# Optimization experiments

Measured on AMD Instinct MI355X. Metric: run time of the kernel, lower is better.

Reference implementation:

```python
import jax, jax.numpy as jnp
import numpy as np

E, H, I, T = 8, 1024, 2816, 512
E4M3_MAX = 448.0  # torch.finfo(float8_e4m3fn).max


def _quantize_to_fp8(w):
    # per-tensor dynamic scaling, identical to quantize_to_fp8 in the source
    amax = jnp.max(jnp.abs(w))
    scale = jnp.maximum(amax / E4M3_MAX, 1e-12)
    fp8 = (w / scale).astype(jnp.float8_e4m3fn)
    return fp8, scale.reshape(1).astype(jnp.float32)


def setup_inputs() -> dict:
    key = jax.random.key(0)
    k1, k2, k3, k4 = jax.random.split(key, 4)
    x = jax.random.normal(k1, (T, H), jnp.float32)
    expert_idx = jax.random.randint(k2, (T,), 0, E)
    # learned 3D expert params (stored compressed as fp8 + per-tensor scale)
    w_gu = jax.random.normal(k3, (E, 2 * I, H), jnp.float32) * 0.02
    w_d = jax.random.normal(k4, (E, H, I), jnp.float32) * 0.02
    w_gu_fp8, w_gu_scale = _quantize_to_fp8(w_gu)
    w_d_fp8, w_d_scale = _quantize_to_fp8(w_d)
    return {
        "x": x,
        "expert_idx": expert_idx,
        "w_gu_fp8": w_gu_fp8,
        "w_gu_scale": w_gu_scale,
        "w_d_fp8": w_d_fp8,
        "w_d_scale": w_d_scale,
    }


def reference(x, expert_idx, w_gu_fp8, w_gu_scale, w_d_fp8, w_d_scale):
    # materialize(): dequantize fp8 -> high precision (fp8.to(dtype) * scale)
    w_gu = w_gu_fp8.astype(jnp.float32) * w_gu_scale  # [E, 2I, H]
    w_d = w_d_fp8.astype(jnp.float32) * w_d_scale     # [E, H, I]
    # inner experts forward: SwiGLU MLP per expert, top-1 routed tokens
    gu = jnp.einsum('th,efh->tef', x, w_gu)            # [T, E, 2I]
    gate, up = jnp.split(gu, 2, axis=-1)               # [T, E, I] each
    h = jax.nn.silu(gate) * up                          # [T, E, I]
    y = jnp.einsum('tei,ehi->teh', h, w_d)              # [T, E, H]
    out = y[jnp.arange(x.shape[0]), expert_idx]         # [T, H] select routed expert
    return out
```

## Files before the change

### kernel.cpp

```cpp
#include <hip/hip_runtime.h>
#include <hip/hip_bf16.h>
#include <stdint.h>

#define E_ 8
#define H_ 1024
#define I_ 2816
#define T_ 512

typedef __attribute__((ext_vector_type(4))) float f32x4;
typedef __attribute__((ext_vector_type(8))) short short8;

typedef __attribute__((address_space(1))) const unsigned GAS;
typedef __attribute__((address_space(3))) unsigned LAS;

__device__ __forceinline__ void dma16(const void* g, void* l) {
    __builtin_amdgcn_global_load_lds((GAS*)g, (LAS*)l, 16, 0, 0);
}
__device__ __forceinline__ unsigned short f2bf(float f) {
    return __builtin_bit_cast(unsigned short, __float2bfloat16(f));
}
__device__ __forceinline__ uint32_t pack_rne(float lo, float hi) {
    return (uint32_t)f2bf(lo) | ((uint32_t)f2bf(hi) << 16);
}
__device__ __forceinline__ uint32_t pack_trunc(float lo, float hi) {
    return (__builtin_bit_cast(uint32_t, hi) & 0xFFFF0000u) |
           (__builtin_bit_cast(uint32_t, lo) >> 16);
}

#define VM2() asm volatile("s_waitcnt vmcnt(2)" ::: "memory")
#define VM6() asm volatile("s_waitcnt vmcnt(6)" ::: "memory")
#define VM0() asm volatile("s_waitcnt vmcnt(0)" ::: "memory")

__global__ __launch_bounds__(256) void route_cvt(const float* __restrict__ x,
                                                 const int* __restrict__ idx,
                                                 int* __restrict__ counts,
                                                 int* __restrict__ bucket,
                                                 unsigned short* __restrict__ xg) {
    int tid = threadIdx.x;
    if (blockIdx.x == 0) {
        if (tid < E_) counts[tid] = 0;
        for (int i = tid; i < E_ * T_; i += 256) bucket[i] = 0;
        __syncthreads();
#pragma unroll
        for (int k = 0; k < 2; ++k) {
            int t = tid + k * 256;
            int e = idx[t];
            int pos = atomicAdd(counts + e, 1);
            bucket[e * T_ + pos] = t;
        }
    }
    int unit = blockIdx.x * 256 + tid;
    const float* xp = x + (size_t)unit * 8;
    float4 a = *(const float4*)xp, b = *(const float4*)(xp + 4);
    uint4 o = make_uint4(pack_rne(a.x, a.y), pack_rne(a.z, a.w),
                         pack_rne(b.x, b.y), pack_rne(b.z, b.w));
    *(uint4*)(xg + (size_t)unit * 8) = o;
}

__global__ __launch_bounds__(256) void gemm1(const unsigned short* __restrict__ xg,
                                             const float* __restrict__ wgu,
                                             const float* __restrict__ sgu_p,
                                             const int* __restrict__ counts,
                                             const int* __restrict__ bucket,
                                             __hip_bfloat16* __restrict__ hbuf) {
    int e = blockIdx.x;
    int f0 = blockIdx.y * 16;
    int cnt = counts[e];

    __shared__ __align__(16) char smem[56 * 1024 + 512];
    int* tok = (int*)(smem + 56 * 1024);
    int tid = threadIdx.x, w = tid >> 6, lane = tid & 63;
    int r16 = lane & 15, kg = lane >> 4;

    if (tid < 128) tok[tid] = bucket[e * T_ + tid];
    __syncthreads();

    const char* xb = (const char*)xg;
    const char* srcA[4]; char* dstA[4];
#pragma unroll
    for (int i = 0; i < 4; ++i) {
        int U = (w * 4 + i) * 64 + lane;
        int t_ = U >> 3, sl = U & 7;
        srcA[i] = xb + (size_t)tok[t_] * 2048 + ((sl ^ (t_ & 7)) * 16);
        dstA[i] = smem + (w * 4 + i) * 1024;
    }
    const char* wbase = (const char*)wgu + (size_t)e * 2 * (size_t)I_ * H_ * 4;
    const char* srcB[2]; char* dstB[2];
#pragma unroll
    for (int i = 0; i < 2; ++i) {
        int U = (w * 2 + i) * 64 + lane;
        int row = U >> 4, sl = U & 15;
        int wr = (row < 16) ? (f0 + row) : (I_ + f0 + row - 16);
        srcB[i] = wbase + (size_t)wr * 4096 + ((sl ^ (row & 15)) * 16);
        dstB[i] = smem + 32 * 1024 + (w * 2 + i) * 1024;
    }

#pragma unroll
    for (int i = 0; i < 2; ++i) dma16(srcB[i], dstB[i]);
#pragma unroll
    for (int i = 0; i < 4; ++i) dma16(srcA[i], dstA[i]);
#pragma unroll
    for (int i = 0; i < 2; ++i) dma16(srcB[i] + 256, dstB[i] + 8192);

    f32x4 accg[2], accu[2];
#pragma unroll
    for (int m = 0; m < 2; ++m) { accg[m] = (f32x4){0,0,0,0}; accu[m] = (f32x4){0,0,0,0}; }

    for (int t = 0; t < 16; ++t) {
        VM2();
        __builtin_amdgcn_sched_barrier(0);
        __builtin_amdgcn_s_barrier();
        int sa = (t + 1 < 16) ? t + 1 : 15;
        int sb = (t + 2 < 16) ? t + 2 : 15;
#pragma unroll
        for (int i = 0; i < 4; ++i)
            dma16(srcA[i] + (size_t)sa * 128, dstA[i] + ((t + 1) & 1) * 16384);
#pragma unroll
        for (int i = 0; i < 2; ++i)
            dma16(srcB[i] + (size_t)sb * 256, dstB[i] + ((t + 2) % 3) * 8192);

        const char* Ab = smem + (t & 1) * 16384;
        const char* Bb = smem + 32 * 1024 + (t % 3) * 8192;
#pragma unroll
        for (int kk = 0; kk < 2; ++kk) {
            int s0 = kk * 8 + kg * 2;
            float4 g0 = *(const float4*)(Bb + r16 * 256 + ((s0 ^ r16) * 16));
            float4 g1 = *(const float4*)(Bb + r16 * 256 + (((s0 + 1) ^ r16) * 16));
            float4 u0 = *(const float4*)(Bb + (16 + r16) * 256 + ((s0 ^ r16) * 16));
            float4 u1 = *(const float4*)(Bb + (16 + r16) * 256 + (((s0 + 1) ^ r16) * 16));
            uint4 bg = make_uint4(pack_trunc(g0.x, g0.y), pack_trunc(g0.z, g0.w),
                                  pack_trunc(g1.x, g1.y), pack_trunc(g1.z, g1.w));
            uint4 bu = make_uint4(pack_trunc(u0.x, u0.y), pack_trunc(u0.z, u0.w),
                                  pack_trunc(u1.x, u1.y), pack_trunc(u1.z, u1.w));
            short8 Bg = __builtin_bit_cast(short8, bg);
            short8 Bu = __builtin_bit_cast(short8, bu);
#pragma unroll
            for (int m = 0; m < 2; ++m) {
                int tr = w * 32 + m * 16 + r16;
                short8 A = *(const short8*)(Ab + tr * 128 + (((kk * 4 + kg) ^ (tr & 7)) * 16));
                accg[m] = __builtin_amdgcn_mfma_f32_16x16x32_bf16(A, Bg, accg[m], 0, 0, 0);
                accu[m] = __builtin_amdgcn_mfma_f32_16x16x32_bf16(A, Bu, accu[m], 0, 0, 0);
            }
        }
    }

    float sgu = sgu_p[0];
#pragma unroll
    for (int m = 0; m < 2; ++m)
#pragma unroll
        for (int j = 0; j < 4; ++j) {
            int tk = w * 32 + m * 16 + kg * 4 + j;
            if (tk < cnt) {
                float g = accg[m][j] * sgu;
                float u = accu[m][j] * sgu;
                float hv = (g / (1.f + __expf(-g))) * u;
                hbuf[(size_t)tok[tk] * I_ + f0 + r16] = __float2bfloat16(hv);
            }
        }
}

__global__ __launch_bounds__(256) void gemm2(const __hip_bfloat16* __restrict__ hbuf,
                                             const float* __restrict__ wd,
                                             const float* __restrict__ sd_p,
                                             const int* __restrict__ counts,
                                             const int* __restrict__ bucket,
                                             float* __restrict__ out) {
    int e = blockIdx.x >> 1, mt = blockIdx.x & 1;
    int cnt = counts[e];
    if (mt * 64 >= cnt) return;
    int h0 = blockIdx.y * 16;

    __shared__ __align__(16) char smem[72 * 1024 + 256];
    int* tok = (int*)(smem + 72 * 1024);
    int tid = threadIdx.x, w = tid >> 6, lane = tid & 63;
    int r16 = lane & 15, kg = lane >> 4;

    float sd = sd_p[0];
    asm volatile("" :: "v"(sd));

    if (tid < 64) tok[tid] = bucket[e * T_ + mt * 64 + tid];
    __syncthreads();

    const char* hb = (const char*)hbuf;
    const char* srcA[4]; char* dstA[4];
#pragma unroll
    for (int i = 0; i < 4; ++i) {
        int U = (w * 4 + i) * 64 + lane;
        int row = U >> 4, sl = U & 15;
        srcA[i] = hb + (size_t)tok[row] * (I_ * 2) + (size_t)((sl ^ (row & 15)) * 16);
        dstA[i] = smem + (w * 4 + i) * 1024;
    }
    const char* wd_e = (const char*)(wd + (size_t)e * (size_t)H_ * I_);
    const char* srcB[2]; char* dstB[2];
#pragma unroll
    for (int i = 0; i < 2; ++i) {
        int U = (w * 2 + i) * 64 + lane;
        int row = U >> 5, sl = U & 31;
        srcB[i] = wd_e + (size_t)(h0 + row) * ((size_t)I_ * 4) + (size_t)((sl ^ (row & 15)) * 16);
        dstB[i] = smem + 48 * 1024 + (w * 2 + i) * 1024;
    }

#define G2_ISSUE(s, buf)                                                     \
    do {                                                                     \
        _Pragma("unroll")                                                    \
        for (int i = 0; i < 4; ++i) dma16(srcA[i] + (size_t)(s) * 256, dstA[i] + (buf) * 16384); \
        _Pragma("unroll")                                                    \
        for (int i = 0; i < 2; ++i) dma16(srcB[i] + (size_t)(s) * 512, dstB[i] + (buf) * 8192);  \
    } while (0)

    G2_ISSUE(0, 0);
    G2_ISSUE(1, 1);

    f32x4 acc = (f32x4){0, 0, 0, 0};

    for (int t = 0; t < 22; ++t) {
        VM6();
        __builtin_amdgcn_s_barrier();
        int tp = (t + 2 < 22) ? t + 2 : 21;
        G2_ISSUE(tp, (t + 2) % 3);
        const char* Ab = smem + (t % 3) * 16384;
        const char* Bb = smem + 48 * 1024 + (t % 3) * 8192;
#pragma unroll
        for (int kk = 0; kk < 4; ++kk) {
            int bo = r16 * 512 + kk * 128 + kg * 32;
            int sw = r16 << 4;
            float4 b0 = *(float4*)(Bb + (bo ^ sw));
            float4 b1 = *(float4*)(Bb + ((bo + 16) ^ sw));
            uint4 bu = make_uint4(pack_trunc(b0.x, b0.y), pack_trunc(b0.z, b0.w),
                                  pack_trunc(b1.x, b1.y), pack_trunc(b1.z, b1.w));
            short8 B = __builtin_bit_cast(short8, bu);
            int ar = w * 16 + r16;
            short8 A = *(short8*)(Ab + ((ar * 256 + kk * 64 + kg * 16) ^ ((ar & 15) << 4)));
            acc = __builtin_amdgcn_mfma_f32_16x16x32_bf16(A, B, acc, 0, 0, 0);
        }
    }
    VM0();

#pragma unroll
    for (int j = 0; j < 4; ++j) {
        int tr = w * 16 + kg * 4 + j;
        int pos = mt * 64 + tr;
        if (pos < cnt)
            out[(size_t)tok[tr] * H_ + h0 + r16] = acc[j] * sd;
    }
#undef G2_ISSUE
}

extern "C" void kernel_launch(void* const* d_in, const int* in_sizes, int n_in,
                              void* d_out, int out_size, void* d_ws, size_t ws_size,
                              hipStream_t stream) {
    const float* x    = (const float*)d_in[0];
    const int*   eidx = (const int*)d_in[1];
    const float* wgu  = (const float*)d_in[2];
    const float* sgu  = (const float*)d_in[3];
    const float* wd   = (const float*)d_in[4];
    const float* sd   = (const float*)d_in[5];
    float* out = (float*)d_out;

    char* ws = (char*)d_ws;
    int* counts = (int*)ws;
    int* bucket = (int*)(ws + 1024);
    unsigned short* xg = (unsigned short*)(ws + 32768);
    __hip_bfloat16* hbuf = (__hip_bfloat16*)(ws + 1114112);

    route_cvt<<<256, 256, 0, stream>>>(x, eidx, counts, bucket, xg);
    gemm1<<<dim3(E_, I_ / 16), 256, 0, stream>>>(xg, wgu, sgu, counts, bucket, hbuf);
    gemm2<<<dim3(E_ * 2, H_ / 16), 256, 0, stream>>>(hbuf, wd, sd, counts, bucket, out);
}
```

Baseline: 113.8 us.

## Restructure gemm1: stage full weight tile once, read activations directly, halve feature tile

```diff
diff --git a/kernel.cpp b/kernel.cpp
--- a/kernel.cpp
+++ b/kernel.cpp
@@ -27,8 +27,10 @@
            (__builtin_bit_cast(uint32_t, lo) >> 16);
 }
 
+#define SB()  __builtin_amdgcn_sched_barrier(0)
+#define VM6() asm volatile("s_waitcnt vmcnt(6)" ::: "memory")
 #define VM2() asm volatile("s_waitcnt vmcnt(2)" ::: "memory")
-#define VM6() asm volatile("s_waitcnt vmcnt(6)" ::: "memory")
+#define VM1() asm volatile("s_waitcnt vmcnt(1)" ::: "memory")
 #define VM0() asm volatile("s_waitcnt vmcnt(0)" ::: "memory")
 
 __global__ __launch_bounds__(256) void route_cvt(const float* __restrict__ x,
@@ -64,99 +66,75 @@
                                              const int* __restrict__ bucket,
                                              __hip_bfloat16* __restrict__ hbuf) {
     int e = blockIdx.x;
-    int f0 = blockIdx.y * 16;
+    int f0 = blockIdx.y * 8;
     int cnt = counts[e];
 
-    __shared__ __align__(16) char smem[56 * 1024 + 512];
-    int* tok = (int*)(smem + 56 * 1024);
+    __shared__ __align__(16) char smem[44 * 1024 + 512];
+    int* tok = (int*)(smem + 44 * 1024);
     int tid = threadIdx.x, w = tid >> 6, lane = tid & 63;
     int r16 = lane & 15, kg = lane >> 4;
 
     if (tid < 128) tok[tid] = bucket[e * T_ + tid];
+
+    const char* gbase = (const char*)wgu + ((size_t)e * 2 * I_ + f0) * H_ * 4;
+    const char* ubase = (const char*)wgu + ((size_t)e * 2 * I_ + I_ + f0) * H_ * 4;
+    char* stage = smem + 32 * 1024;
+    int soff = w * 1024 + lane * 16;
+
+#define P1SRC(c) ((((c) < 8) ? (gbase + (size_t)(c) * 4096) : (ubase + (size_t)((c) - 8) * 4096)) + soff)
+#define P1DST(c) (stage + ((c) % 3) * 4096 + soff)
+    dma16(P1SRC(0), P1DST(0));
+    dma16(P1SRC(1), P1DST(1));
+    dma16(P1SRC(2), P1DST(2));
+
+    for (int c = 0; c < 16; ++c) {
+        if (c <= 13) { VM2(); } else if (c == 14) { VM1(); } else { VM0(); }
+        SB();
+        float4 v = *(const float4*)(stage + (c % 3) * 4096 + tid * 16);
+        uint2 o; o.x = pack_trunc(v.x, v.y); o.y = pack_trunc(v.z, v.w);
+        *(uint2*)(smem + c * 2048 + (((tid >> 1) ^ (c & 7)) * 16) + (tid & 1) * 8) = o;
+        SB();
+        if (c + 3 < 16) dma16(P1SRC(c + 3), P1DST(c + 3));
+    }
     __syncthreads();
 
-    const char* xb = (const char*)xg;
-    const char* srcA[4]; char* dstA[4];
-#pragma unroll
-    for (int i = 0; i < 4; ++i) {
-        int U = (w * 4 + i) * 64 + lane;
-        int t_ = U >> 3, sl = U & 7;
-        srcA[i] = xb + (size_t)tok[t_] * 2048 + ((sl ^ (t_ & 7)) * 16);
-        dstA[i] = smem + (w * 4 + i) * 1024;
-    }
-    const char* wbase = (const char*)wgu + (size_t)e * 2 * (size_t)I_ * H_ * 4;
-    const char* srcB[2]; char* dstB[2];
-#pragma unroll
-    for (int i = 0; i < 2; ++i) {
-        int U = (w * 2 + i) * 64 + lane;
-        int row = U >> 4, sl = U & 15;
-        int wr = (row < 16) ? (f0 + row) : (I_ + f0 + row - 16);
-        srcB[i] = wbase + (size_t)wr * 4096 + ((sl ^ (row & 15)) * 16);
-        dstB[i] = smem + 32 * 1024 + (w * 2 + i) * 1024;
-    }
-
-#pragma unroll
-    for (int i = 0; i < 2; ++i) dma16(srcB[i], dstB[i]);
-#pragma unroll
-    for (int i = 0; i < 4; ++i) dma16(srcA[i], dstA[i]);
-#pragma unroll
-    for (int i = 0; i < 2; ++i) dma16(srcB[i] + 256, dstB[i] + 8192);
-
-    f32x4 accg[2], accu[2];
-#pragma unroll
-    for (int m = 0; m < 2; ++m) { accg[m] = (f32x4){0,0,0,0}; accu[m] = (f32x4){0,0,0,0}; }
-
+    const char* a0p = (const char*)xg + (size_t)tok[w * 32 + r16] * 2048 + kg * 16;
+    const char* a1p = (const char*)xg + (size_t)tok[w * 32 + 16 + r16] * 2048 + kg * 16;
+
+    f32x4 acc[2];
+    acc[0] = (f32x4){0, 0, 0, 0};
+    acc[1] = (f32x4){0, 0, 0, 0};
+
+#pragma unroll 4
     for (int t = 0; t < 16; ++t) {
-        VM2();
-        __builtin_amdgcn_sched_barrier(0);
-        __builtin_amdgcn_s_barrier();
-        int sa = (t + 1 < 16) ? t + 1 : 15;
-        int sb = (t + 2 < 16) ? t + 2 : 15;
-#pragma unroll
-        for (int i = 0; i < 4; ++i)
-            dma16(srcA[i] + (size_t)sa * 128, dstA[i] + ((t + 1) & 1) * 16384);
-#pragma unroll
-        for (int i = 0; i < 2; ++i)
-            dma16(srcB[i] + (size_t)sb * 256, dstB[i] + ((t + 2) % 3) * 8192);
-
-        const char* Ab = smem + (t & 1) * 16384;
-        const char* Bb = smem + 32 * 1024 + (t % 3) * 8192;
 #pragma unroll
         for (int kk = 0; kk < 2; ++kk) {
-            int s0 = kk * 8 + kg * 2;
-            float4 g0 = *(const float4*)(Bb + r16 * 256 + ((s0 ^ r16) * 16));
-            float4 g1 = *(const float4*)(Bb + r16 * 256 + (((s0 + 1) ^ r16) * 16));
-            float4 u0 = *(const float4*)(Bb + (16 + r16) * 256 + ((s0 ^ r16) * 16));
-            float4 u1 = *(const float4*)(Bb + (16 + r16) * 256 + (((s0 + 1) ^ r16) * 16));
-            uint4 bg = make_uint4(pack_trunc(g0.x, g0.y), pack_trunc(g0.z, g0.w),
-                                  pack_trunc(g1.x, g1.y), pack_trunc(g1.z, g1.w));
-            uint4 bu = make_uint4(pack_trunc(u0.x, u0.y), pack_trunc(u0.z, u0.w),
-                                  pack_trunc(u1.x, u1.y), pack_trunc(u1.z, u1.w));
-            short8 Bg = __builtin_bit_cast(short8, bg);
-            short8 Bu = __builtin_bit_cast(short8, bu);
-#pragma unroll
-            for (int m = 0; m < 2; ++m) {
-                int tr = w * 32 + m * 16 + r16;
-                short8 A = *(const short8*)(Ab + tr * 128 + (((kk * 4 + kg) ^ (tr & 7)) * 16));
-                accg[m] = __builtin_amdgcn_mfma_f32_16x16x32_bf16(A, Bg, accg[m], 0, 0, 0);
-                accu[m] = __builtin_amdgcn_mfma_f32_16x16x32_bf16(A, Bu, accu[m], 0, 0, 0);
+            short8 Bf = *(const short8*)(smem + r16 * 2048 +
+                         (((t * 8 + kk * 4 + kg) ^ (r16 & 7)) * 16));
+            short8 A0 = *(const short8*)(a0p + t * 128 + kk * 64);
+            short8 A1 = *(const short8*)(a1p + t * 128 + kk * 64);
+            acc[0] = __builtin_amdgcn_mfma_f32_16x16x32_bf16(A0, Bf, acc[0], 0, 0, 0);
+            acc[1] = __builtin_amdgcn_mfma_f32_16x16x32_bf16(A1, Bf, acc[1], 0, 0, 0);
+        }
+    }
+
+    float sgu = sgu_p[0];
+#pragma unroll
+    for (int m = 0; m < 2; ++m)
+#pragma unroll
+        for (int j = 0; j < 4; ++j) {
+            float self = acc[m][j] * sgu;
+            float other = __shfl_xor(self, 8);
+            if (r16 < 8) {
+                float g = self, u = other;
+                float hv = (g / (1.f + __expf(-g))) * u;
+                int tk = w * 32 + m * 16 + kg * 4 + j;
+                if (tk < cnt)
+                    hbuf[(size_t)tok[tk] * I_ + f0 + r16] = __float2bfloat16(hv);
             }
         }
-    }
-
-    float sgu = sgu_p[0];
-#pragma unroll
-    for (int m = 0; m < 2; ++m)
-#pragma unroll
-        for (int j = 0; j < 4; ++j) {
-            int tk = w * 32 + m * 16 + kg * 4 + j;
-            if (tk < cnt) {
-                float g = accg[m][j] * sgu;
-                float u = accu[m][j] * sgu;
-                float hv = (g / (1.f + __expf(-g))) * u;
-                hbuf[(size_t)tok[tk] * I_ + f0 + r16] = __float2bfloat16(hv);
-            }
-        }
+#undef P1SRC
+#undef P1DST
 }
 
 __global__ __launch_bounds__(256) void gemm2(const __hip_bfloat16* __restrict__ hbuf,
@@ -264,6 +242,6 @@
     __hip_bfloat16* hbuf = (__hip_bfloat16*)(ws + 1114112);
 
     route_cvt<<<256, 256, 0, stream>>>(x, eidx, counts, bucket, xg);
-    gemm1<<<dim3(E_, I_ / 16), 256, 0, stream>>>(xg, wgu, sgu, counts, bucket, hbuf);
+    gemm1<<<dim3(E_, I_ / 8), 256, 0, stream>>>(xg, wgu, sgu, counts, bucket, hbuf);
     gemm2<<<dim3(E_ * 2, H_ / 16), 256, 0, stream>>>(hbuf, wd, sd, counts, bucket, out);
 }
```

Result: slower. 153.6 us (+35.0%).
